# Kernel tuning notes

Hardware: AMD Instinct MI355X
Metric: run time of the kernel (lower is better)

## Reference

```python
import jax, jax.numpy as jnp
import numpy as np

N = 4096      # number of stocks (token axis)
D = 512       # d_model
H = 8         # nhead
DE = 64       # d_emb
DH = D // H   # head_dim = 64
TEMP = float(np.sqrt(DH))
EPS = 1e-5


def _ln(x, g, b):
    mu = jnp.mean(x, axis=-1, keepdims=True)
    var = jnp.var(x, axis=-1, keepdims=True)
    return (x - mu) * jax.lax.rsqrt(var + EPS) * g + b


def setup_inputs() -> dict:
    key = jax.random.key(0)
    ks = jax.random.split(key, 8)
    init = lambda k, shape, fan: (jax.random.normal(k, shape, jnp.float32) / np.sqrt(fan).astype(np.float32))
    return {
        "x": jax.random.normal(ks[0], (N, D), jnp.float32),
        "industry_emb": jax.random.normal(ks[1], (N, DE), jnp.float32),
        # projection weights stored as [in, out] so y = x @ W
        "Wq": init(ks[2], (D + DE, D), D + DE),
        "Wk": init(ks[3], (D + DE, D), D + DE),
        "Wv": init(ks[4], (D, D), D),
        "g1": jnp.ones((D,), jnp.float32), "b1": jnp.zeros((D,), jnp.float32),
        "g2": jnp.ones((DE,), jnp.float32), "b2": jnp.zeros((DE,), jnp.float32),
        "g3": jnp.ones((D,), jnp.float32), "b3": jnp.zeros((D,), jnp.float32),
        "W_ffn1": init(ks[5], (D, D), D), "b_ffn1": jnp.zeros((D,), jnp.float32),
        "W_ffn2": init(ks[6], (D, D), D), "b_ffn2": jnp.zeros((D,), jnp.float32),
    }


def reference(x, industry_emb, Wq, Wk, Wv, g1, b1, g2, b2, g3, b3,
              W_ffn1, b_ffn1, W_ffn2, b_ffn2):
    xn = _ln(x, g1, b1)                       # [N, D]
    en = _ln(industry_emb, g2, b2)            # [N, DE]
    qk_in = jnp.concatenate([xn, en], axis=-1)  # [N, D+DE]
    q = (qk_in @ Wq).reshape(N, H, DH)
    k = (qk_in @ Wk).reshape(N, H, DH)
    v = (xn @ Wv).reshape(N, H, DH)
    # batched multi-head attention (equivalent to the per-head torch loop)
    scores = jnp.einsum('nhd,mhd->hnm', q, k) / TEMP   # [H, N, N]
    attn = jax.nn.softmax(scores, axis=-1)
    att = jnp.einsum('hnm,mhd->nhd', attn, v).reshape(N, D)
    xt = xn + att
    h = _ln(xt, g3, b3)
    ffn = jax.nn.relu(h @ W_ffn1 + b_ffn1) @ W_ffn2 + b_ffn2
    return xt + ffn
```

## Files before the change

### kernel.cpp

```cpp
#include <hip/hip_runtime.h>

#define NTOK 4096
#define DMODEL 512
#define DEMB 64
#define DCAT 576
#define NHEAD 8
#define DHEAD 64
#define QSCALE 0.18033688011112042f

typedef float f32x4 __attribute__((ext_vector_type(4)));
typedef float f32x16 __attribute__((ext_vector_type(16)));
typedef short s16x8 __attribute__((ext_vector_type(8)));
typedef unsigned short u16;
typedef u16 u16x4 __attribute__((ext_vector_type(4)));
typedef u16 u16x8 __attribute__((ext_vector_type(8)));
typedef unsigned int u32;

__device__ __forceinline__ u16 f2bf(float f) {
  union { float f; unsigned u; } v; v.f = f;
  unsigned r = v.u + 0x7fffu + ((v.u >> 16) & 1u);
  return (u16)(r >> 16);
}

__device__ __forceinline__ float bf2f(u16 u) {
  union { unsigned u; float f; } v; v.u = ((unsigned)u) << 16;
  return v.f;
}

__device__ __forceinline__ u32 cvtpk_bf16(float lo, float hi) {
  u32 r;
  asm("v_cvt_pk_bf16_f32 %0, %1, %2" : "=v"(r) : "v"(lo), "v"(hi));
  return r;
}

__device__ __forceinline__ void gload16(const void* g, void* lds) {
  __builtin_amdgcn_global_load_lds((const __attribute__((address_space(1))) u32*)g,
                                   (__attribute__((address_space(3))) u32*)lds, 16, 0, 0);
}

__global__ void wtrans_kernel(const float* __restrict__ Wq, const float* __restrict__ Wk,
                              const float* __restrict__ Wv, const float* __restrict__ Wf1,
                              const float* __restrict__ Wf2,
                              u16* __restrict__ Tqkv, u16* __restrict__ Tf1, u16* __restrict__ Tf2) {
  __shared__ float tile[64][65];
  int w = blockIdx.z;
  const float* src; u16* dst; int Ksrc, Kdst;
  if (w == 0)      { src = Wq;  dst = Tqkv;              Ksrc = 576; Kdst = 576; }
  else if (w == 1) { src = Wk;  dst = Tqkv + 512 * 576;  Ksrc = 576; Kdst = 576; }
  else if (w == 2) { src = Wv;  dst = Tqkv + 1024 * 576; Ksrc = 512; Kdst = 576; }
  else if (w == 3) { src = Wf1; dst = Tf1;               Ksrc = 512; Kdst = 512; }
  else             { src = Wf2; dst = Tf2;               Ksrc = 512; Kdst = 512; }
  int kb = blockIdx.x * 64;
  if (kb >= Kdst) return;
  int nb = blockIdx.y * 64;
  int tid = threadIdx.x;
  #pragma unroll
  for (int i = 0; i < 16; ++i) {
    int idx = tid + i * 256;
    int r = idx >> 6, c = idx & 63;
    tile[r][c] = (kb + r < Ksrc) ? src[(size_t)(kb + r) * DMODEL + nb + c] : 0.0f;
  }
  __syncthreads();
  #pragma unroll
  for (int i = 0; i < 16; ++i) {
    int idx = tid + i * 256;
    int r = idx >> 6, c = idx & 63;
    dst[(size_t)(nb + r) * Kdst + kb + c] = f2bf(tile[c][r]);
  }
}

__global__ void lnx_kernel(const float* __restrict__ x, const float* __restrict__ g,
                           const float* __restrict__ b, float* __restrict__ xt,
                           u16* __restrict__ qkin) {
  int row = blockIdx.x * 4 + (threadIdx.x >> 6);
  int lane = threadIdx.x & 63;
  const float* xr = x + (size_t)row * DMODEL + lane * 8;
  float v[8];
  float4 a0 = *(const float4*)xr;
  float4 a1 = *(const float4*)(xr + 4);
  v[0]=a0.x; v[1]=a0.y; v[2]=a0.z; v[3]=a0.w; v[4]=a1.x; v[5]=a1.y; v[6]=a1.z; v[7]=a1.w;
  float s = 0.f, ss = 0.f;
  #pragma unroll
  for (int j = 0; j < 8; ++j) { s += v[j]; ss += v[j]*v[j]; }
  #pragma unroll
  for (int off = 32; off > 0; off >>= 1) { s += __shfl_xor(s, off); ss += __shfl_xor(ss, off); }
  float mu = s * (1.0f / DMODEL);
  float var = ss * (1.0f / DMODEL) - mu * mu;
  float rs = rsqrtf(var + 1e-5f);
  float4 g0 = *(const float4*)(g + lane * 8);
  float4 g1v = *(const float4*)(g + lane * 8 + 4);
  float4 b0 = *(const float4*)(b + lane * 8);
  float4 b1v = *(const float4*)(b + lane * 8 + 4);
  float gg[8] = {g0.x,g0.y,g0.z,g0.w,g1v.x,g1v.y,g1v.z,g1v.w};
  float bb[8] = {b0.x,b0.y,b0.z,b0.w,b1v.x,b1v.y,b1v.z,b1v.w};
  float o[8]; u16x8 ob;
  #pragma unroll
  for (int j = 0; j < 8; ++j) { o[j] = (v[j]-mu)*rs*gg[j] + bb[j]; ob[j] = f2bf(o[j]); }
  float* xo = xt + (size_t)row * DMODEL + lane * 8;
  *(float4*)xo = make_float4(o[0],o[1],o[2],o[3]);
  *(float4*)(xo + 4) = make_float4(o[4],o[5],o[6],o[7]);
  *(u16x8*)(qkin + (size_t)row * DCAT + lane * 8) = ob;
}

__global__ void lne_kernel(const float* __restrict__ e, const float* __restrict__ g,
                           const float* __restrict__ b, u16* __restrict__ qkin) {
  int row = blockIdx.x * 4 + (threadIdx.x >> 6);
  int lane = threadIdx.x & 63;
  float v = e[(size_t)row * DEMB + lane];
  float s = v, ss = v * v;
  #pragma unroll
  for (int off = 32; off > 0; off >>= 1) { s += __shfl_xor(s, off); ss += __shfl_xor(ss, off); }
  float mu = s * (1.0f / DEMB);
  float var = ss * (1.0f / DEMB) - mu * mu;
  float rs = rsqrtf(var + 1e-5f);
  float o = (v - mu) * rs * g[lane] + b[lane];
  qkin[(size_t)row * DCAT + DMODEL + lane] = f2bf(o);
}

__global__ void ln3_kernel(float* __restrict__ xt, const float* __restrict__ g,
                           const float* __restrict__ b, u16* __restrict__ hb,
                           const u16* __restrict__ obuf, const float* __restrict__ lbuf) {
  int row = blockIdx.x * 4 + (threadIdx.x >> 6);
  int lane = threadIdx.x & 63;
  int h = lane >> 3;
  int dh0 = (lane & 7) * 8;
  float* xr = xt + (size_t)row * DMODEL + lane * 8;
  float v[8];
  float4 a0 = *(const float4*)xr;
  float4 a1 = *(const float4*)(xr + 4);
  v[0]=a0.x; v[1]=a0.y; v[2]=a0.z; v[3]=a0.w; v[4]=a1.x; v[5]=a1.y; v[6]=a1.z; v[7]=a1.w;
  float osum[8] = {};
  float lsum = 0.f;
  #pragma unroll
  for (int s = 0; s < 4; ++s) {
    size_t hb_idx = (size_t)(s * 8 + h) * NTOK + row;
    u16x8 ov = *(const u16x8*)(obuf + hb_idx * 64 + dh0);
    lsum += lbuf[hb_idx];
    #pragma unroll
    for (int j = 0; j < 8; ++j) osum[j] += bf2f(ov[j]);
  }
  float rcpl = 1.0f / lsum;
  #pragma unroll
  for (int j = 0; j < 8; ++j) v[j] += osum[j] * rcpl;
  *(float4*)xr = make_float4(v[0],v[1],v[2],v[3]);
  *(float4*)(xr + 4) = make_float4(v[4],v[5],v[6],v[7]);
  float s = 0.f, ss = 0.f;
  #pragma unroll
  for (int j = 0; j < 8; ++j) { s += v[j]; ss += v[j]*v[j]; }
  #pragma unroll
  for (int off = 32; off > 0; off >>= 1) { s += __shfl_xor(s, off); ss += __shfl_xor(ss, off); }
  float mu = s * (1.0f / DMODEL);
  float var = ss * (1.0f / DMODEL) - mu * mu;
  float rs = rsqrtf(var + 1e-5f);
  float4 g0 = *(const float4*)(g + lane * 8);
  float4 g1v = *(const float4*)(g + lane * 8 + 4);
  float4 b0 = *(const float4*)(b + lane * 8);
  float4 b1v = *(const float4*)(b + lane * 8 + 4);
  float gg[8] = {g0.x,g0.y,g0.z,g0.w,g1v.x,g1v.y,g1v.z,g1v.w};
  float bb[8] = {b0.x,b0.y,b0.z,b0.w,b1v.x,b1v.y,b1v.z,b1v.w};
  u16x8 ob;
  #pragma unroll
  for (int j = 0; j < 8; ++j) ob[j] = f2bf((v[j]-mu)*rs*gg[j] + bb[j]);
  *(u16x8*)(hb + (size_t)row * DMODEL + lane * 8) = ob;
}

template<int MODE>
__global__ __launch_bounds__(256) void gemm_kernel(
    const u16* __restrict__ A, int lda, const u16* __restrict__ Bt, int K,
    u16* __restrict__ outb, float* __restrict__ outf,
    const float* __restrict__ bias, const float* __restrict__ xt) {
  __shared__ __align__(16) u16 smem[8192];
  u16* Al = smem;
  u16* Bl = smem + 4096;
  int tid = threadIdx.x, lane = tid & 63, wid = tid >> 6;
  int li = lane & 15, g4 = lane >> 4;
  int n0 = blockIdx.x * 64, m0 = blockIdx.y * 64;
  int wr = (wid >> 1) * 32, wc = (wid & 1) * 32;
  f32x4 acc[2][2] = {};
  for (int k0 = 0; k0 < K; k0 += 64) {
    #pragma unroll
    for (int i = 0; i < 2; ++i) {
      int idx = i * 256 + tid;
      int row = idx >> 3, cb = (idx & 7) * 8;
      gload16(A + (size_t)(m0 + row) * lda + k0 + cb, (char*)Al + idx * 16);
    }
    #pragma unroll
    for (int i = 0; i < 2; ++i) {
      int idx = i * 256 + tid;
      int row = idx >> 3, cb = (idx & 7) * 8;
      gload16(Bt + (size_t)(n0 + row) * K + k0 + cb, (char*)Bl + idx * 16);
    }
    __syncthreads();
    #pragma unroll
    for (int kk = 0; kk < 2; ++kk) {
      s16x8 af[2], bfv[2];
      #pragma unroll
      for (int mi = 0; mi < 2; ++mi)
        af[mi] = *(const s16x8*)&Al[(wr + mi * 16 + li) * 64 + kk * 32 + g4 * 8];
      #pragma unroll
      for (int ni = 0; ni < 2; ++ni)
        bfv[ni] = *(const s16x8*)&Bl[(wc + ni * 16 + li) * 64 + kk * 32 + g4 * 8];
      #pragma unroll
      for (int mi = 0; mi < 2; ++mi)
        #pragma unroll
        for (int ni = 0; ni < 2; ++ni)
          acc[mi][ni] = __builtin_amdgcn_mfma_f32_16x16x32_bf16(af[mi], bfv[ni], acc[mi][ni], 0, 0, 0);
    }
    __syncthreads();
  }
  if (MODE == 0) {
    if (n0 < 1024) {
      float scale = (n0 < 512) ? QSCALE : 1.0f;
      int nb = (n0 < 512) ? n0 : n0 - 512;
      u16* dst = outb + ((n0 < 512) ? 0 : (size_t)NTOK * DMODEL);
      #pragma unroll
      for (int mi = 0; mi < 2; ++mi)
        #pragma unroll
        for (int ni = 0; ni < 2; ++ni) {
          int col = nb + wc + ni * 16 + li;
          int h = col >> 6, dh = col & 63;
          #pragma unroll
          for (int r = 0; r < 4; ++r) {
            int row = m0 + wr + mi * 16 + g4 * 4 + r;
            dst[((size_t)h * NTOK + row) * DHEAD + dh] = f2bf(acc[mi][ni][r] * scale);
          }
        }
    } else {
      u16* vT = outb + (size_t)2 * NTOK * DMODEL;
      u16* tp = smem;
      __syncthreads();
      #pragma unroll
      for (int mi = 0; mi < 2; ++mi)
        #pragma unroll
        for (int ni = 0; ni < 2; ++ni) {
          int cl = wc + ni * 16 + li;
          int r0 = wr + mi * 16 + g4 * 4;
          int r0p = (r0 & ~12) | ((r0 & 4) << 1) | ((r0 & 8) >> 1);
          u16x4 pk;
          pk[0] = f2bf(acc[mi][ni][0]); pk[1] = f2bf(acc[mi][ni][1]);
          pk[2] = f2bf(acc[mi][ni][2]); pk[3] = f2bf(acc[mi][ni][3]);
          *(u16x4*)&tp[cl * 80 + r0p] = pk;
        }
      __syncthreads();
      for (int c = tid; c < 512; c += 256) {
        int cl = c >> 3, seg = c & 7;
        u16x8 v = *(const u16x8*)&tp[cl * 80 + seg * 8];
        *(u16x8*)&vT[(size_t)(n0 - 1024 + cl) * NTOK + m0 + seg * 8] = v;
      }
    }
  } else {
    #pragma unroll
    for (int mi = 0; mi < 2; ++mi)
      #pragma unroll
      for (int ni = 0; ni < 2; ++ni) {
        int col = n0 + wc + ni * 16 + li;
        float bv = bias[col];
        #pragma unroll
        for (int r = 0; r < 4; ++r) {
          int row = m0 + wr + mi * 16 + g4 * 4 + r;
          float v = acc[mi][ni][r] + bv;
          if (MODE == 3) {
            v = fmaxf(v, 0.0f);
            outb[(size_t)row * DMODEL + col] = f2bf(v);
          } else {
            outf[(size_t)row * DMODEL + col] = v + xt[(size_t)row * DMODEL + col];
          }
        }
      }
  }
}

__global__ __launch_bounds__(256, 2) void attn_kernel(
    const u16* __restrict__ qh, const u16* __restrict__ kh,
    const u16* __restrict__ vT, u16* __restrict__ obuf, float* __restrict__ lbuf) {
  __shared__ __align__(16) u16 kbufT[2][4096];
  __shared__ __align__(16) u16 vbufT[2][4096];
  int tid = threadIdx.x, lane = tid & 63, w = tid >> 6;
  int lq = lane & 31, h5 = lane >> 5;
  int h = blockIdx.x & 7, ks = (blockIdx.x >> 3) & 3, qt = blockIdx.x >> 5;
  int q0w = qt * 128 + w * 32;
  int ko0 = ks * 1024;
  const u16* qb = qh + ((size_t)h * NTOK + q0w + lq) * DHEAD;
  s16x8 qf[4];
  #pragma unroll
  for (int kc = 0; kc < 4; ++kc)
    qf[kc] = *(const s16x8*)(qb + kc * 16 + h5 * 8);
  f32x16 o[2] = {};
  float lsum = 0.f;
  const char* kh_b = (const char*)(kh + (size_t)h * NTOK * DHEAD);
  const char* v_b = (const char*)(vT + (size_t)h * DHEAD * NTOK);

  auto stage = [&](int c, int ko) {
    #pragma unroll
    for (int i = 0; i < 2; ++i) {
      int s = tid + i * 256;
      int lo6 = s & 63, r6 = s >> 6;
      gload16(kh_b + (size_t)(ko + lo6) * 128 + r6 * 16, (char*)&kbufT[c][0] + s * 16);
      gload16(v_b + (size_t)lo6 * (NTOK * 2) + (size_t)(ko + r6 * 8) * 2,
              (char*)&vbufT[c][0] + s * 16);
    }
  };

  stage(0, ko0);
  asm volatile("s_waitcnt vmcnt(0)" ::: "memory");
  __builtin_amdgcn_sched_barrier(0);
  __syncthreads();

  for (int t = 0; t < 16; ++t) {
    int cur = t & 1;
    if (t < 15) stage(cur ^ 1, ko0 + (t + 1) * 64);
    const u16* Kl = &kbufT[cur][0];
    const u16* Vl = &vbufT[cur][0];
    #pragma unroll
    for (int kb2 = 0; kb2 < 2; ++kb2) {
      f32x16 st = {};
      #pragma unroll
      for (int kc = 0; kc < 4; ++kc) {
        s16x8 kf = *(const s16x8*)(Kl + ((kc * 2 + h5) * 64 + kb2 * 32 + lq) * 8);
        st = __builtin_amdgcn_mfma_f32_32x32x16_bf16(kf, qf[kc], st, 0, 0, 0);
      }
      float p[16];
      #pragma unroll
      for (int r = 0; r < 16; ++r) { p[r] = __builtin_amdgcn_exp2f(st[r]); lsum += p[r]; }
      #pragma unroll
      for (int cl = 0; cl < 2; ++cl) {
        int b = cl * 8;
        union { u32 wv[4]; s16x8 hv; } pu;
        pu.wv[0] = cvtpk_bf16(p[b + 0], p[b + 1]);
        pu.wv[1] = cvtpk_bf16(p[b + 2], p[b + 3]);
        pu.wv[2] = cvtpk_bf16(p[b + 4], p[b + 5]);
        pu.wv[3] = cvtpk_bf16(p[b + 6], p[b + 7]);
        int kcg = kb2 * 2 + cl;
        #pragma unroll
        for (int dhalf = 0; dhalf < 2; ++dhalf) {
          s16x8 bv = *(const s16x8*)(Vl + ((kcg * 2 + h5) * 64 + dhalf * 32 + lq) * 8);
          o[dhalf] = __builtin_amdgcn_mfma_f32_32x32x16_bf16(pu.hv, bv, o[dhalf], 0, 0, 0);
        }
      }
    }
    if (t < 15) {
      asm volatile("s_waitcnt vmcnt(0)" ::: "memory");
      __builtin_amdgcn_sched_barrier(0);
      __syncthreads();
    }
  }

  lsum += __shfl_xor(lsum, 32);
  size_t slice = (size_t)(ks * 8 + h) * NTOK;
  if (h5 == 0) lbuf[slice + q0w + lq] = lsum;
  u16* ob = obuf + (slice + q0w) * 64;
  #pragma unroll
  for (int dhalf = 0; dhalf < 2; ++dhalf)
    #pragma unroll
    for (int r = 0; r < 16; ++r) {
      int crow = (r & 3) + 8 * (r >> 2) + 4 * h5;
      ob[(size_t)crow * 64 + dhalf * 32 + lq] = f2bf(o[dhalf][r]);
    }
}

extern "C" void kernel_launch(void* const* d_in, const int* in_sizes, int n_in,
                              void* d_out, int out_size, void* d_ws, size_t ws_size,
                              hipStream_t stream) {
  const float* x   = (const float*)d_in[0];
  const float* emb = (const float*)d_in[1];
  const float* Wq  = (const float*)d_in[2];
  const float* Wk  = (const float*)d_in[3];
  const float* Wv  = (const float*)d_in[4];
  const float* g1  = (const float*)d_in[5];
  const float* b1  = (const float*)d_in[6];
  const float* g2  = (const float*)d_in[7];
  const float* b2  = (const float*)d_in[8];
  const float* g3  = (const float*)d_in[9];
  const float* b3  = (const float*)d_in[10];
  const float* Wf1 = (const float*)d_in[11];
  const float* bf1 = (const float*)d_in[12];
  const float* Wf2 = (const float*)d_in[13];
  const float* bf2 = (const float*)d_in[14];
  float* out = (float*)d_out;

  char* ws = (char*)d_ws;
  size_t off = 0;
  auto alloc = [&](size_t bytes) { void* p = ws + off; off += (bytes + 255) & ~255ull; return p; };
  float* xt = (float*)alloc((size_t)NTOK * DMODEL * 4);
  u16* qkin = (u16*)alloc((size_t)NTOK * DCAT * 2);
  u16* hb   = (u16*)alloc((size_t)NTOK * DMODEL * 2);
  u16* r1   = (u16*)alloc((size_t)NTOK * DMODEL * 2);
  u16* qkvh = (u16*)alloc((size_t)3 * NTOK * DMODEL * 2);
  u16* Tqkv = (u16*)alloc((size_t)1536 * DCAT * 2);
  u16* Tf1  = (u16*)alloc((size_t)DMODEL * DMODEL * 2);
  u16* Tf2  = (u16*)alloc((size_t)DMODEL * DMODEL * 2);
  u16* obuf = (u16*)alloc((size_t)4 * NHEAD * NTOK * DHEAD * 2);
  float* lbuf = (float*)alloc((size_t)4 * NHEAD * NTOK * 4);
  u16* qhd = qkvh;
  u16* khd = qkvh + (size_t)NTOK * DMODEL;
  u16* vTd = qkvh + (size_t)2 * NTOK * DMODEL;

  wtrans_kernel<<<dim3(9, 8, 5), 256, 0, stream>>>(Wq, Wk, Wv, Wf1, Wf2, Tqkv, Tf1, Tf2);
  lnx_kernel<<<1024, 256, 0, stream>>>(x, g1, b1, xt, qkin);
  lne_kernel<<<1024, 256, 0, stream>>>(emb, g2, b2, qkin);
  gemm_kernel<0><<<dim3(24, 64), 256, 0, stream>>>(qkin, DCAT, Tqkv, DCAT, qkvh, nullptr, nullptr, nullptr);
  attn_kernel<<<1024, 256, 0, stream>>>(qhd, khd, vTd, obuf, lbuf);
  ln3_kernel<<<1024, 256, 0, stream>>>(xt, g3, b3, hb, obuf, lbuf);
  gemm_kernel<3><<<dim3(8, 64), 256, 0, stream>>>(hb, DMODEL, Tf1, DMODEL, r1, nullptr, bf1, nullptr);
  gemm_kernel<4><<<dim3(8, 64), 256, 0, stream>>>(r1, DMODEL, Tf2, DMODEL, nullptr, out, bf2, xt);
}
```

Before: 110.7 us.

## Enlarge QKV GEMM tiles and double attention block size for K/V reuse

Adds a dedicated QKV projection GEMM with 128x64 tiles (4x2 MFMA fragments per wave), halving the grid and reusing each B tile across twice as many rows. The attention kernel moves to 512-thread blocks covering 256 queries, so each staged K/V chunk in LDS serves eight waves instead of four and each thread issues one load per stage. This cuts global/L2 traffic for K/V and weights, at the cost of fewer blocks, launch bounds of one block per CU, and more registers in the GEMM.

```diff
diff --git a/kernel.cpp b/kernel.cpp
--- a/kernel.cpp
+++ b/kernel.cpp
@@ -164,6 +164,88 @@
   *(u16x8*)(hb + (size_t)row * DMODEL + lane * 8) = ob;
 }
 
+__global__ __launch_bounds__(256) void gemm_qkv_kernel(
+    const u16* __restrict__ A, const u16* __restrict__ Bt, u16* __restrict__ outb) {
+  __shared__ __align__(16) u16 smem[12288];
+  u16* Al = smem;
+  u16* Bl = smem + 8192;
+  int tid = threadIdx.x, lane = tid & 63, wid = tid >> 6;
+  int li = lane & 15, g4 = lane >> 4;
+  int n0 = blockIdx.x * 64, m0 = blockIdx.y * 128;
+  int wr = (wid >> 1) * 64, wc = (wid & 1) * 32;
+  f32x4 acc[4][2] = {};
+  for (int k0 = 0; k0 < DCAT; k0 += 64) {
+    #pragma unroll
+    for (int i = 0; i < 4; ++i) {
+      int idx = i * 256 + tid;
+      int row = idx >> 3, cb = (idx & 7) * 8;
+      gload16(A + (size_t)(m0 + row) * DCAT + k0 + cb, (char*)Al + idx * 16);
+    }
+    #pragma unroll
+    for (int i = 0; i < 2; ++i) {
+      int idx = i * 256 + tid;
+      int row = idx >> 3, cb = (idx & 7) * 8;
+      gload16(Bt + (size_t)(n0 + row) * DCAT + k0 + cb, (char*)Bl + idx * 16);
+    }
+    __syncthreads();
+    #pragma unroll
+    for (int kk = 0; kk < 2; ++kk) {
+      s16x8 af[4], bfv[2];
+      #pragma unroll
+      for (int mi = 0; mi < 4; ++mi)
+        af[mi] = *(const s16x8*)&Al[(wr + mi * 16 + li) * 64 + kk * 32 + g4 * 8];
+      #pragma unroll
+      for (int ni = 0; ni < 2; ++ni)
+        bfv[ni] = *(const s16x8*)&Bl[(wc + ni * 16 + li) * 64 + kk * 32 + g4 * 8];
+      #pragma unroll
+      for (int mi = 0; mi < 4; ++mi)
+        #pragma unroll
+        for (int ni = 0; ni < 2; ++ni)
+          acc[mi][ni] = __builtin_amdgcn_mfma_f32_16x16x32_bf16(af[mi], bfv[ni], acc[mi][ni], 0, 0, 0);
+    }
+    __syncthreads();
+  }
+  if (n0 < 1024) {
+    float scale = (n0 < 512) ? QSCALE : 1.0f;
+    int nb = (n0 < 512) ? n0 : n0 - 512;
+    u16* dst = outb + ((n0 < 512) ? 0 : (size_t)NTOK * DMODEL);
+    #pragma unroll
+    for (int mi = 0; mi < 4; ++mi)
+      #pragma unroll
+      for (int ni = 0; ni < 2; ++ni) {
+        int col = nb + wc + ni * 16 + li;
+        int h = col >> 6, dh = col & 63;
+        #pragma unroll
+        for (int r = 0; r < 4; ++r) {
+          int row = m0 + wr + mi * 16 + g4 * 4 + r;
+          dst[((size_t)h * NTOK + row) * DHEAD + dh] = f2bf(acc[mi][ni][r] * scale);
+        }
+      }
+  } else {
+    u16* vT = outb + (size_t)2 * NTOK * DMODEL;
+    u16* tp = smem;
+    __syncthreads();
+    #pragma unroll
+    for (int mi = 0; mi < 4; ++mi)
+      #pragma unroll
+      for (int ni = 0; ni < 2; ++ni) {
+        int cl = wc + ni * 16 + li;
+        int r0 = wr + mi * 16 + g4 * 4;
+        int r0p = (r0 & ~12) | ((r0 & 4) << 1) | ((r0 & 8) >> 1);
+        u16x4 pk;
+        pk[0] = f2bf(acc[mi][ni][0]); pk[1] = f2bf(acc[mi][ni][1]);
+        pk[2] = f2bf(acc[mi][ni][2]); pk[3] = f2bf(acc[mi][ni][3]);
+        *(u16x4*)&tp[cl * 136 + r0p] = pk;
+      }
+    __syncthreads();
+    for (int c = tid; c < 1024; c += 256) {
+      int cl = c >> 4, seg = c & 15;
+      u16x8 v = *(const u16x8*)&tp[cl * 136 + seg * 8];
+      *(u16x8*)&vT[(size_t)(n0 - 1024 + cl) * NTOK + m0 + seg * 8] = v;
+    }
+  }
+}
+
 template<int MODE>
 __global__ __launch_bounds__(256) void gemm_kernel(
     const u16* __restrict__ A, int lda, const u16* __restrict__ Bt, int K,
@@ -208,69 +290,27 @@
     }
     __syncthreads();
   }
-  if (MODE == 0) {
-    if (n0 < 1024) {
-      float scale = (n0 < 512) ? QSCALE : 1.0f;
-      int nb = (n0 < 512) ? n0 : n0 - 512;
-      u16* dst = outb + ((n0 < 512) ? 0 : (size_t)NTOK * DMODEL);
-      #pragma unroll
-      for (int mi = 0; mi < 2; ++mi)
-        #pragma unroll
-        for (int ni = 0; ni < 2; ++ni) {
-          int col = nb + wc + ni * 16 + li;
-          int h = col >> 6, dh = col & 63;
-          #pragma unroll
-          for (int r = 0; r < 4; ++r) {
-            int row = m0 + wr + mi * 16 + g4 * 4 + r;
-            dst[((size_t)h * NTOK + row) * DHEAD + dh] = f2bf(acc[mi][ni][r] * scale);
-          }
-        }
-    } else {
-      u16* vT = outb + (size_t)2 * NTOK * DMODEL;
-      u16* tp = smem;
-      __syncthreads();
-      #pragma unroll
-      for (int mi = 0; mi < 2; ++mi)
-        #pragma unroll
-        for (int ni = 0; ni < 2; ++ni) {
-          int cl = wc + ni * 16 + li;
-          int r0 = wr + mi * 16 + g4 * 4;
-          int r0p = (r0 & ~12) | ((r0 & 4) << 1) | ((r0 & 8) >> 1);
-          u16x4 pk;
-          pk[0] = f2bf(acc[mi][ni][0]); pk[1] = f2bf(acc[mi][ni][1]);
-          pk[2] = f2bf(acc[mi][ni][2]); pk[3] = f2bf(acc[mi][ni][3]);
-          *(u16x4*)&tp[cl * 80 + r0p] = pk;
-        }
-      __syncthreads();
-      for (int c = tid; c < 512; c += 256) {
-        int cl = c >> 3, seg = c & 7;
-        u16x8 v = *(const u16x8*)&tp[cl * 80 + seg * 8];
-        *(u16x8*)&vT[(size_t)(n0 - 1024 + cl) * NTOK + m0 + seg * 8] = v;
-      }
-    }
-  } else {
-    #pragma unroll
-    for (int mi = 0; mi < 2; ++mi)
-      #pragma unroll
-      for (int ni = 0; ni < 2; ++ni) {
-        int col = n0 + wc + ni * 16 + li;
-        float bv = bias[col];
-        #pragma unroll
-        for (int r = 0; r < 4; ++r) {
-          int row = m0 + wr + mi * 16 + g4 * 4 + r;
-          float v = acc[mi][ni][r] + bv;
-          if (MODE == 3) {
-            v = fmaxf(v, 0.0f);
-            outb[(size_t)row * DMODEL + col] = f2bf(v);
-          } else {
-            outf[(size_t)row * DMODEL + col] = v + xt[(size_t)row * DMODEL + col];
-          }
+  #pragma unroll
+  for (int mi = 0; mi < 2; ++mi)
+    #pragma unroll
+    for (int ni = 0; ni < 2; ++ni) {
+      int col = n0 + wc + ni * 16 + li;
+      float bv = bias[col];
+      #pragma unroll
+      for (int r = 0; r < 4; ++r) {
+        int row = m0 + wr + mi * 16 + g4 * 4 + r;
+        float v = acc[mi][ni][r] + bv;
+        if (MODE == 3) {
+          v = fmaxf(v, 0.0f);
+          outb[(size_t)row * DMODEL + col] = f2bf(v);
+        } else {
+          outf[(size_t)row * DMODEL + col] = v + xt[(size_t)row * DMODEL + col];
         }
       }
-  }
-}
-
-__global__ __launch_bounds__(256, 2) void attn_kernel(
+    }
+}
+
+__global__ __launch_bounds__(512, 1) void attn_kernel(
     const u16* __restrict__ qh, const u16* __restrict__ kh,
     const u16* __restrict__ vT, u16* __restrict__ obuf, float* __restrict__ lbuf) {
   __shared__ __align__(16) u16 kbufT[2][4096];
@@ -278,7 +318,7 @@
   int tid = threadIdx.x, lane = tid & 63, w = tid >> 6;
   int lq = lane & 31, h5 = lane >> 5;
   int h = blockIdx.x & 7, ks = (blockIdx.x >> 3) & 3, qt = blockIdx.x >> 5;
-  int q0w = qt * 128 + w * 32;
+  int q0w = qt * 256 + w * 32;
   int ko0 = ks * 1024;
   const u16* qb = qh + ((size_t)h * NTOK + q0w + lq) * DHEAD;
   s16x8 qf[4];
@@ -291,14 +331,10 @@
   const char* v_b = (const char*)(vT + (size_t)h * DHEAD * NTOK);
 
   auto stage = [&](int c, int ko) {
-    #pragma unroll
-    for (int i = 0; i < 2; ++i) {
-      int s = tid + i * 256;
-      int lo6 = s & 63, r6 = s >> 6;
-      gload16(kh_b + (size_t)(ko + lo6) * 128 + r6 * 16, (char*)&kbufT[c][0] + s * 16);
-      gload16(v_b + (size_t)lo6 * (NTOK * 2) + (size_t)(ko + r6 * 8) * 2,
-              (char*)&vbufT[c][0] + s * 16);
-    }
+    int lo6 = tid & 63, r6 = tid >> 6;
+    gload16(kh_b + (size_t)(ko + lo6) * 128 + r6 * 16, (char*)&kbufT[c][0] + tid * 16);
+    gload16(v_b + (size_t)lo6 * (NTOK * 2) + (size_t)(ko + r6 * 8) * 2,
+            (char*)&vbufT[c][0] + tid * 16);
   };
 
   stage(0, ko0);
@@ -398,8 +434,8 @@
   wtrans_kernel<<<dim3(9, 8, 5), 256, 0, stream>>>(Wq, Wk, Wv, Wf1, Wf2, Tqkv, Tf1, Tf2);
   lnx_kernel<<<1024, 256, 0, stream>>>(x, g1, b1, xt, qkin);
   lne_kernel<<<1024, 256, 0, stream>>>(emb, g2, b2, qkin);
-  gemm_kernel<0><<<dim3(24, 64), 256, 0, stream>>>(qkin, DCAT, Tqkv, DCAT, qkvh, nullptr, nullptr, nullptr);
-  attn_kernel<<<1024, 256, 0, stream>>>(qhd, khd, vTd, obuf, lbuf);
+  gemm_qkv_kernel<<<dim3(24, 32), 256, 0, stream>>>(qkin, Tqkv, qkvh);
+  attn_kernel<<<512, 512, 0, stream>>>(qhd, khd, vTd, obuf, lbuf);
   ln3_kernel<<<1024, 256, 0, stream>>>(xt, g3, b3, hb, obuf, lbuf);
   gemm_kernel<3><<<dim3(8, 64), 256, 0, stream>>>(hb, DMODEL, Tf1, DMODEL, r1, nullptr, bf1, nullptr);
   gemm_kernel<4><<<dim3(8, 64), 256, 0, stream>>>(r1, DMODEL, Tf2, DMODEL, nullptr, out, bf2, xt);
```

New measurement: 102.2 us. -7.7%, faster.
